# Performance work log

Hardware: AMD Instinct MI355X
Metric: run time of the kernel (lower is better)

## Reference

```python
import jax, jax.numpy as jnp
import numpy as np
from jax import lax

EPS = 1e-8


def setup_inputs() -> dict:
    key = jax.random.key(0)
    k1, k2, k3, k4, k5 = jax.random.split(key, 5)
    b, c_in, c_out, h, w_sp, k, z = 8, 256, 256, 128, 128, 3, 512
    return {
        "x": jax.random.normal(k1, (b, c_in, h, w_sp), dtype=jnp.float32),
        "w": jax.random.normal(k2, (b, z), dtype=jnp.float32),
        "weight": jax.random.normal(k3, (c_out, c_in, k, k), dtype=jnp.float32),
        "affine_w": jax.random.normal(k4, (c_in, z), dtype=jnp.float32) * 0.02,
        "affine_b": jax.random.normal(k5, (c_in,), dtype=jnp.float32) * 0.02,
    }


def reference(x, w, weight, affine_w, affine_b):
    # style: [b, c_in] -> broadcast over (out_ch, kh, kw); +1 as in StyleGAN2
    style = w @ affine_w.T + affine_b + 1.0                      # [b, c_in]
    wgt = weight[None] * style[:, None, :, None, None]           # [b, O, I, kh, kw]
    # demodulation
    denom = lax.rsqrt(jnp.sum(wgt * wgt, axis=(2, 3, 4)) + EPS)  # [b, O]
    wgt = wgt * denom[:, :, None, None, None]

    # per-sample conv (equivalent to groups=b grouped conv), 'same' padding
    def conv_one(xi, wi):
        # xi: [I, H, W], wi: [O, I, kh, kw]
        return lax.conv_general_dilated(
            xi[None], wi, window_strides=(1, 1), padding="SAME",
            dimension_numbers=("NCHW", "OIHW", "NCHW"))[0]

    return jax.vmap(conv_one)(x, wgt)                            # [b, O, H, W]
```

## Files before the change

kernel.cpp:

```cpp
#include <hip/hip_runtime.h>

#define EPS 1e-8f

using short8 = __attribute__((ext_vector_type(8))) short;
using f32x4  = __attribute__((ext_vector_type(4))) float;
typedef unsigned short u16;

__device__ __forceinline__ u16 f2bf(float f) {
    union { float f; unsigned u; } v; v.f = f;
    unsigned u = v.u;
    return (u16)((u + 0x7FFFu + ((u >> 16) & 1u)) >> 16);
}

__device__ __forceinline__ void g2l16(const void* gsrc, void* ldst) {
    __builtin_amdgcn_global_load_lds(
        (const __attribute__((address_space(1))) unsigned int*)gsrc,
        (__attribute__((address_space(3))) unsigned int*)ldst, 16, 0, 0);
}

__global__ void style_kernel(const float* __restrict__ w,
                             const float* __restrict__ affine_w,
                             const float* __restrict__ affine_b,
                             float* __restrict__ style) {
    int b = blockIdx.x;
    int i = threadIdx.x;
    __shared__ float wb[512];
    for (int z = threadIdx.x; z < 512; z += 256) wb[z] = w[b * 512 + z];
    __syncthreads();
    const float* aw = affine_w + i * 512;
    float acc = 0.f;
#pragma unroll 4
    for (int z = 0; z < 512; z += 4) {
        float4 a4 = *reinterpret_cast<const float4*>(aw + z);
        acc += a4.x * wb[z] + a4.y * wb[z + 1] + a4.z * wb[z + 2] + a4.w * wb[z + 3];
    }
    style[b * 256 + i] = acc + affine_b[i] + 1.0f;
}

__global__ void modw_kernel(const float* __restrict__ weight,
                            const float* __restrict__ style,
                            u16* __restrict__ wgt) {
    int b = blockIdx.x >> 8;
    int o = blockIdx.x & 255;
    int ic = threadIdx.x;
    float s = style[b * 256 + ic];
    const float* wp = weight + (size_t)(o * 256 + ic) * 9;
    float m[9];
    float ss = 0.f;
#pragma unroll
    for (int t = 0; t < 9; ++t) { m[t] = wp[t] * s; ss += m[t] * m[t]; }
#pragma unroll
    for (int off = 32; off > 0; off >>= 1) ss += __shfl_down(ss, off);
    __shared__ float part[4];
    int lane = threadIdx.x & 63, wid = threadIdx.x >> 6;
    if (lane == 0) part[wid] = ss;
    __syncthreads();
    float denom = rsqrtf(part[0] + part[1] + part[2] + part[3] + EPS);
    int g = ic >> 3, j = ic & 7;
#pragma unroll
    for (int t = 0; t < 9; ++t) {
        size_t idx = ((((size_t)(b * 9 + t) * 32 + g) * 256 + o) << 3) + j;
        wgt[idx] = f2bf(m[t] * denom);
    }
}

__global__ __launch_bounds__(256) void xform_kernel(const float* __restrict__ x,
                                                    u16* __restrict__ xb) {
    int s = blockIdx.x * 256 + threadIdx.x;
    int w = s & 127, h = (s >> 7) & 127, g = (s >> 14) & 31, b = s >> 19;
    const float* xp = x + (((size_t)(b * 256 + g * 8) * 128 + h) * 128 + w);
    union { u16 u[8]; short8 v; } pk;
#pragma unroll
    for (int j = 0; j < 8; ++j) pk.u[j] = f2bf(xp[(size_t)j * 16384]);
    *reinterpret_cast<short8*>(&xb[(size_t)s * 8]) = pk.v;
}

__global__ __launch_bounds__(256, 2) void conv_kernel(
    const u16* __restrict__ xb,
    const u16* __restrict__ wgt,
    float* __restrict__ out) {

    __shared__ __align__(16) u16 Xs[4][4][130][8];
    __shared__ __align__(16) u16 As[2][4][129][8];

    int bid = blockIdx.x;
    int ht = bid & 63;
    int ot = (bid >> 6) & 1;
    int b  = bid >> 7;
    int h0 = ht * 2;

    int tid = threadIdx.x, lane = tid & 63, wid = tid >> 6;
    int wm = wid >> 1, wr = wid & 1;
    int l15 = lane & 15, lg = lane >> 4;

    {
        short8 z = {0, 0, 0, 0, 0, 0, 0, 0};
        short8* xz = reinterpret_cast<short8*>(&Xs[0][0][0][0]);
        for (int i = tid; i < 2080; i += 256) xz[i] = z;
    }

    f32x4 acc[4][8] = {};

    auto stageX = [&](int c) {
        int hr = h0 + wid - 1;
        if ((unsigned)hr < 128u) {
#pragma unroll
            for (int k = 0; k < 8; ++k) {
                int g = k >> 1, half = k & 1;
                const u16* src = xb +
                    ((((size_t)(b * 32 + c * 4 + g) * 128 + hr) * 128) + half * 64 + lane) * 8;
                g2l16(src, &Xs[wid][g][1 + half * 64][0]);
            }
        }
    };
    auto stageA = [&](int nc, int nt, int nb) {
        const u16* base = wgt + ((((size_t)(b * 9 + nt) * 32) + nc * 4 + wid) * 256 + ot * 128) * 8;
        g2l16(base + (size_t)lane * 8, &As[nb][wid][0][0]);
        g2l16(base + (size_t)(64 + lane) * 8, &As[nb][wid][64][0]);
    };

    __syncthreads();
    stageX(0);
    stageA(0, 0, 0);
    __syncthreads();

    int cur = 0;
    for (int c = 0; c < 8; ++c) {
        for (int t = 0; t < 9; ++t) {
            bool lastPhase = (c == 7 && t == 8);
            if (!lastPhase) {
                int nt = t + 1, nc = c;
                if (nt == 9) { nt = 0; nc = c + 1; }
                stageA(nc, nt, cur ^ 1);
            }
            int kh = t / 3, kw = t - kh * 3;
            short8 af[4], bfv[8];
#pragma unroll
            for (int mi = 0; mi < 4; ++mi)
                af[mi] = *reinterpret_cast<const short8*>(&As[cur][lg][wm * 64 + mi * 16 + l15][0]);
#pragma unroll
            for (int ni = 0; ni < 8; ++ni)
                bfv[ni] = *reinterpret_cast<const short8*>(&Xs[wr + kh][lg][ni * 16 + l15 + kw][0]);
#pragma unroll
            for (int mi = 0; mi < 4; ++mi)
#pragma unroll
                for (int ni = 0; ni < 8; ++ni)
                    acc[mi][ni] = __builtin_amdgcn_mfma_f32_16x16x32_bf16(
                        af[mi], bfv[ni], acc[mi][ni], 0, 0, 0);
            if (t == 8 && c < 7) {
                __syncthreads();
                stageX(c + 1);
            }
            if (!lastPhase) __syncthreads();
            cur ^= 1;
        }
    }

    int h = h0 + wr;
#pragma unroll
    for (int mi = 0; mi < 4; ++mi) {
        int o = ot * 128 + wm * 64 + mi * 16 + lg * 4;
#pragma unroll
        for (int ni = 0; ni < 8; ++ni) {
            int w_ = ni * 16 + l15;
            float* op = out + (((size_t)(b * 256 + o) * 128 + h) * 128 + w_);
#pragma unroll
            for (int r = 0; r < 4; ++r)
                op[(size_t)r * 16384] = acc[mi][ni][r];
        }
    }
}

extern "C" void kernel_launch(void* const* d_in, const int* in_sizes, int n_in,
                              void* d_out, int out_size, void* d_ws, size_t ws_size,
                              hipStream_t stream) {
    const float* x        = (const float*)d_in[0];
    const float* w        = (const float*)d_in[1];
    const float* weight   = (const float*)d_in[2];
    const float* affine_w = (const float*)d_in[3];
    const float* affine_b = (const float*)d_in[4];
    float* out = (float*)d_out;

    float* style = (float*)d_ws;
    u16* wgt = (u16*)((char*)d_ws + 8192);
    u16* xbuf = (u16*)((char*)d_ws + 8192 + 9437184);

    xform_kernel<<<16384, 256, 0, stream>>>(x, xbuf);
    style_kernel<<<8, 256, 0, stream>>>(w, affine_w, affine_b, style);
    modw_kernel<<<2048, 256, 0, stream>>>(weight, style, wgt);
    conv_kernel<<<1024, 256, 0, stream>>>(xbuf, wgt, out);
}
```

Before: 202.7 us.

## Restructure conv kernel into 512-thread blocks with triple-buffered weights and double-buffered input

Each conv block now covers all 256 output channels with 8 waves, so every staged input row is reused across twice as many outputs. Weights move through a 3-deep LDS ring and input rows through a double buffer, and explicit vmcnt waits with one barrier per step replace the paired __syncthreads. The changes also add MFMA priority boosting, a block-index swizzle, and redirection of out-of-range row loads into a trash buffer. LDS use rises sharply, which may lower occupancy, and the hand-counted waits could be fragile.

```diff
diff --git a/kernel.cpp b/kernel.cpp
--- a/kernel.cpp
+++ b/kernel.cpp
@@ -5,6 +5,12 @@
 using short8 = __attribute__((ext_vector_type(8))) short;
 using f32x4  = __attribute__((ext_vector_type(4))) float;
 typedef unsigned short u16;
+
+#define WAITV(N) asm volatile("s_waitcnt vmcnt(" #N ")" ::: "memory")
+#define WAITLGKM0() do { asm volatile("s_waitcnt lgkmcnt(0)" ::: "memory"); \
+                         __builtin_amdgcn_sched_barrier(0); } while (0)
+#define BARRIER() do { __builtin_amdgcn_s_barrier(); \
+                       asm volatile("" ::: "memory"); } while (0)
 
 __device__ __forceinline__ u16 f2bf(float f) {
     union { float f; unsigned u; } v; v.f = f;
@@ -75,91 +81,103 @@
     *reinterpret_cast<short8*>(&xb[(size_t)s * 8]) = pk.v;
 }
 
-__global__ __launch_bounds__(256, 2) void conv_kernel(
+__global__ __launch_bounds__(512, 2) void conv_kernel(
     const u16* __restrict__ xb,
     const u16* __restrict__ wgt,
     float* __restrict__ out) {
 
-    __shared__ __align__(16) u16 Xs[4][4][130][8];
-    __shared__ __align__(16) u16 As[2][4][129][8];
+    __shared__ __align__(16) u16 Xs[2][4][4][130][8];
+    __shared__ __align__(16) u16 As[3][4][256][8];
+    __shared__ __align__(16) u16 trash[512];
 
     int bid = blockIdx.x;
-    int ht = bid & 63;
-    int ot = (bid >> 6) & 1;
-    int b  = bid >> 7;
+    int swz = (bid & 7) * 64 + (bid >> 3);
+    int ht = swz & 63, b = swz >> 6;
     int h0 = ht * 2;
 
     int tid = threadIdx.x, lane = tid & 63, wid = tid >> 6;
     int wm = wid >> 1, wr = wid & 1;
     int l15 = lane & 15, lg = lane >> 4;
 
+    auto stageA = [&](int p, int ring) {
+        int t = p % 9, c = p / 9;
+        const u16* wbase = wgt + ((size_t)(b * 9 + t) * 32 + c * 4) * (256 * 8);
+#pragma unroll
+        for (int k = 0; k < 2; ++k) {
+            int seg = wid * 2 + k, g = seg >> 2, oq = seg & 3;
+            const u16* src = wbase + ((size_t)g * 256 + oq * 64 + lane) * 8;
+            g2l16(src, &As[ring][g][oq * 64][0]);
+        }
+    };
+    auto stageX = [&](int c1, int bx) {
+        int row = wid >> 1;
+        int hr = h0 + row - 1;
+        bool oob = ((unsigned)hr >= 128u);
+        int hc = oob ? 0 : hr;
+#pragma unroll
+        for (int k = 0; k < 4; ++k) {
+            int g = (wid * 2 + (k >> 1)) & 3, half = k & 1;
+            const u16* src = xb +
+                ((((size_t)(b * 32 + c1 * 4 + g)) * 128 + hc) * 128 + half * 64 + lane) * 8;
+            void* dst = oob ? (void*)trash : (void*)&Xs[bx][row][g][1 + half * 64][0];
+            g2l16(src, dst);
+        }
+    };
+
     {
         short8 z = {0, 0, 0, 0, 0, 0, 0, 0};
-        short8* xz = reinterpret_cast<short8*>(&Xs[0][0][0][0]);
-        for (int i = tid; i < 2080; i += 256) xz[i] = z;
-    }
+        short8* p0 = reinterpret_cast<short8*>(&Xs[0][0][0][0][0]);
+        for (int i = tid; i < 4160; i += 512) p0[i] = z;
+    }
+    __syncthreads();
+
+    stageX(0, 0);
+    stageA(0, 0);
+    stageA(1, 1);
+    WAITV(2);
+    BARRIER();
 
     f32x4 acc[4][8] = {};
 
-    auto stageX = [&](int c) {
-        int hr = h0 + wid - 1;
-        if ((unsigned)hr < 128u) {
-#pragma unroll
-            for (int k = 0; k < 8; ++k) {
-                int g = k >> 1, half = k & 1;
-                const u16* src = xb +
-                    ((((size_t)(b * 32 + c * 4 + g) * 128 + hr) * 128) + half * 64 + lane) * 8;
-                g2l16(src, &Xs[wid][g][1 + half * 64][0]);
-            }
-        }
-    };
-    auto stageA = [&](int nc, int nt, int nb) {
-        const u16* base = wgt + ((((size_t)(b * 9 + nt) * 32) + nc * 4 + wid) * 256 + ot * 128) * 8;
-        g2l16(base + (size_t)lane * 8, &As[nb][wid][0][0]);
-        g2l16(base + (size_t)(64 + lane) * 8, &As[nb][wid][64][0]);
-    };
-
-    __syncthreads();
-    stageX(0);
-    stageA(0, 0, 0);
-    __syncthreads();
-
-    int cur = 0;
     for (int c = 0; c < 8; ++c) {
         for (int t = 0; t < 9; ++t) {
-            bool lastPhase = (c == 7 && t == 8);
-            if (!lastPhase) {
-                int nt = t + 1, nc = c;
-                if (nt == 9) { nt = 0; nc = c + 1; }
-                stageA(nc, nt, cur ^ 1);
-            }
+            int p = c * 9 + t;
+            if (t == 0 && c < 7) stageX(c + 1, (c + 1) & 1);
+            if (p <= 69) stageA(p + 2, (p + 2) % 3);
+
+            int ring = p % 3;
             int kh = t / 3, kw = t - kh * 3;
-            short8 af[4], bfv[8];
+            short8 af[4], bx8[8];
 #pragma unroll
             for (int mi = 0; mi < 4; ++mi)
-                af[mi] = *reinterpret_cast<const short8*>(&As[cur][lg][wm * 64 + mi * 16 + l15][0]);
+                af[mi] = *reinterpret_cast<const short8*>(
+                    &As[ring][lg][wm * 64 + mi * 16 + l15][0]);
 #pragma unroll
             for (int ni = 0; ni < 8; ++ni)
-                bfv[ni] = *reinterpret_cast<const short8*>(&Xs[wr + kh][lg][ni * 16 + l15 + kw][0]);
+                bx8[ni] = *reinterpret_cast<const short8*>(
+                    &Xs[c & 1][wr + kh][lg][ni * 16 + l15 + kw][0]);
+            WAITLGKM0();
+            __builtin_amdgcn_s_setprio(1);
 #pragma unroll
             for (int mi = 0; mi < 4; ++mi)
 #pragma unroll
                 for (int ni = 0; ni < 8; ++ni)
                     acc[mi][ni] = __builtin_amdgcn_mfma_f32_16x16x32_bf16(
-                        af[mi], bfv[ni], acc[mi][ni], 0, 0, 0);
-            if (t == 8 && c < 7) {
-                __syncthreads();
-                stageX(c + 1);
-            }
-            if (!lastPhase) __syncthreads();
-            cur ^= 1;
+                        af[mi], bx8[ni], acc[mi][ni], 0, 0, 0);
+            __builtin_amdgcn_s_setprio(0);
+            __builtin_amdgcn_sched_barrier(0);
+
+            if (t == 0 && c < 7)  { WAITV(6); }
+            else if (p <= 69)     { WAITV(2); }
+            else if (p == 70)     { WAITV(0); }
+            BARRIER();
         }
     }
 
     int h = h0 + wr;
 #pragma unroll
     for (int mi = 0; mi < 4; ++mi) {
-        int o = ot * 128 + wm * 64 + mi * 16 + lg * 4;
+        int o = wm * 64 + mi * 16 + lg * 4;
 #pragma unroll
         for (int ni = 0; ni < 8; ++ni) {
             int w_ = ni * 16 + l15;
@@ -188,5 +206,5 @@
     xform_kernel<<<16384, 256, 0, stream>>>(x, xbuf);
     style_kernel<<<8, 256, 0, stream>>>(w, affine_w, affine_b, style);
     modw_kernel<<<2048, 256, 0, stream>>>(weight, style, wgt);
-    conv_kernel<<<1024, 256, 0, stream>>>(xbuf, wgt, out);
-}
+    conv_kernel<<<512, 512, 0, stream>>>(xbuf, wgt, out);
+}
```

New measurement: 219.4 us. 1.08x slower.

## Drop LDS staging in conv; load fragments directly from padded global buffers

Applied to the files above, without the earlier changes.

The input transform now writes a zero-padded bf16 layout with halo rows and columns. The conv kernel loads MFMA operand fragments straight from global memory into registers, double-buffered one tap ahead, instead of staging through LDS with barriers. Each block now covers one output row for all 256 output channels, uses a swizzled block index, and raises wave priority around the MFMA loop. This removes LDS traffic and __syncthreads, at the cost of redundant global/L2 reads and more register pressure.

```diff
diff --git a/kernel.cpp b/kernel.cpp
--- a/kernel.cpp
+++ b/kernel.cpp
@@ -10,12 +10,6 @@
     union { float f; unsigned u; } v; v.f = f;
     unsigned u = v.u;
     return (u16)((u + 0x7FFFu + ((u >> 16) & 1u)) >> 16);
-}
-
-__device__ __forceinline__ void g2l16(const void* gsrc, void* ldst) {
-    __builtin_amdgcn_global_load_lds(
-        (const __attribute__((address_space(1))) unsigned int*)gsrc,
-        (__attribute__((address_space(3))) unsigned int*)ldst, 16, 0, 0);
 }
 
 __global__ void style_kernel(const float* __restrict__ w,
@@ -66,13 +60,20 @@
 
 __global__ __launch_bounds__(256) void xform_kernel(const float* __restrict__ x,
                                                     u16* __restrict__ xb) {
+    int r = blockIdx.y;
     int s = blockIdx.x * 256 + threadIdx.x;
-    int w = s & 127, h = (s >> 7) & 127, g = (s >> 14) & 31, b = s >> 19;
-    const float* xp = x + (((size_t)(b * 256 + g * 8) * 128 + h) * 128 + w);
+    if (s >= 4160) return;
+    int g = s / 130, wp = s - g * 130;
+    short8* dst = reinterpret_cast<short8*>(xb + ((size_t)r * 4160 + s) * 8);
+    short8 z = {0, 0, 0, 0, 0, 0, 0, 0};
+    if (r == 0) { *dst = z; return; }
+    int b = (r - 1) / 129, hh = (r - 1) - b * 129;
+    if (hh == 128 || wp == 0 || wp == 129) { *dst = z; return; }
+    const float* xp = x + (((size_t)(b * 256 + g * 8)) * 128 + hh) * 128 + (wp - 1);
     union { u16 u[8]; short8 v; } pk;
 #pragma unroll
     for (int j = 0; j < 8; ++j) pk.u[j] = f2bf(xp[(size_t)j * 16384]);
-    *reinterpret_cast<short8*>(&xb[(size_t)s * 8]) = pk.v;
+    *dst = pk.v;
 }
 
 __global__ __launch_bounds__(256, 2) void conv_kernel(
@@ -80,86 +81,69 @@
     const u16* __restrict__ wgt,
     float* __restrict__ out) {
 
-    __shared__ __align__(16) u16 Xs[4][4][130][8];
-    __shared__ __align__(16) u16 As[2][4][129][8];
+    int bid = blockIdx.x;
+    int swz = ((bid & 7) << 7) | (bid >> 3);
+    int h = swz & 127, b = swz >> 7;
 
-    int bid = blockIdx.x;
-    int ht = bid & 63;
-    int ot = (bid >> 6) & 1;
-    int b  = bid >> 7;
-    int h0 = ht * 2;
-
-    int tid = threadIdx.x, lane = tid & 63, wid = tid >> 6;
-    int wm = wid >> 1, wr = wid & 1;
+    int tid = threadIdx.x, lane = tid & 63, og = tid >> 6;
     int l15 = lane & 15, lg = lane >> 4;
 
-    {
-        short8 z = {0, 0, 0, 0, 0, 0, 0, 0};
-        short8* xz = reinterpret_cast<short8*>(&Xs[0][0][0][0]);
-        for (int i = tid; i < 2080; i += 256) xz[i] = z;
-    }
+    const int RP = 33280;
+    int lanePartA = lg * 2048 + og * 512 + l15 * 8;
+    int lanePartB = lg * 1040 + l15 * 8;
 
+    short8 af[2][4], bx[2][8];
     f32x4 acc[4][8] = {};
 
-    auto stageX = [&](int c) {
-        int hr = h0 + wid - 1;
-        if ((unsigned)hr < 128u) {
+    auto issueA = [&](int buf, int c, int t) {
+        const u16* ap = wgt + (size_t)((b * 9 + t) * 32 + c * 4) * 2048 + lanePartA;
 #pragma unroll
-            for (int k = 0; k < 8; ++k) {
-                int g = k >> 1, half = k & 1;
-                const u16* src = xb +
-                    ((((size_t)(b * 32 + c * 4 + g) * 128 + hr) * 128) + half * 64 + lane) * 8;
-                g2l16(src, &Xs[wid][g][1 + half * 64][0]);
-            }
-        }
+        for (int mi = 0; mi < 4; ++mi)
+            af[buf][mi] = *reinterpret_cast<const short8*>(ap + mi * 128);
     };
-    auto stageA = [&](int nc, int nt, int nb) {
-        const u16* base = wgt + ((((size_t)(b * 9 + nt) * 32) + nc * 4 + wid) * 256 + ot * 128) * 8;
-        g2l16(base + (size_t)lane * 8, &As[nb][wid][0][0]);
-        g2l16(base + (size_t)(64 + lane) * 8, &As[nb][wid][64][0]);
+    auto issueB = [&](int buf, int c, int t) {
+        int kh = t / 3, kw = t - kh * 3;
+        const u16* bp = xb + (size_t)(b * 129 + h + kh) * RP + c * 4160 +
+                        lanePartB + kw * 8;
+#pragma unroll
+        for (int ni = 0; ni < 8; ++ni)
+            bx[buf][ni] = *reinterpret_cast<const short8*>(bp + ni * 128);
+    };
+    auto domfma = [&](int cur) {
+        __builtin_amdgcn_s_setprio(1);
+#pragma unroll
+        for (int mi = 0; mi < 4; ++mi)
+#pragma unroll
+            for (int ni = 0; ni < 8; ++ni)
+                acc[mi][ni] = __builtin_amdgcn_mfma_f32_16x16x32_bf16(
+                    af[cur][mi], bx[cur][ni], acc[cur == cur ? mi : mi][ni], 0, 0, 0);
+        __builtin_amdgcn_s_setprio(0);
     };
 
-    __syncthreads();
-    stageX(0);
-    stageA(0, 0, 0);
-    __syncthreads();
-
-    int cur = 0;
-    for (int c = 0; c < 8; ++c) {
-        for (int t = 0; t < 9; ++t) {
-            bool lastPhase = (c == 7 && t == 8);
-            if (!lastPhase) {
-                int nt = t + 1, nc = c;
-                if (nt == 9) { nt = 0; nc = c + 1; }
-                stageA(nc, nt, cur ^ 1);
+    issueA(0, 0, 0);
+    issueB(0, 0, 0);
+#pragma unroll 1
+    for (int c2 = 0; c2 < 8; c2 += 2) {
+#pragma unroll
+        for (int tt = 0; tt < 18; ++tt) {
+            int cur = tt & 1;
+            bool last = (c2 == 6) && (tt == 17);
+            if (!last) {
+                int ntt = tt + 1;
+                int nc, nt;
+                if (ntt == 18) { nc = c2 + 2; nt = 0; }
+                else if (ntt >= 9) { nc = c2 + 1; nt = ntt - 9; }
+                else { nc = c2; nt = ntt; }
+                issueA(cur ^ 1, nc, nt);
+                issueB(cur ^ 1, nc, nt);
             }
-            int kh = t / 3, kw = t - kh * 3;
-            short8 af[4], bfv[8];
-#pragma unroll
-            for (int mi = 0; mi < 4; ++mi)
-                af[mi] = *reinterpret_cast<const short8*>(&As[cur][lg][wm * 64 + mi * 16 + l15][0]);
-#pragma unroll
-            for (int ni = 0; ni < 8; ++ni)
-                bfv[ni] = *reinterpret_cast<const short8*>(&Xs[wr + kh][lg][ni * 16 + l15 + kw][0]);
-#pragma unroll
-            for (int mi = 0; mi < 4; ++mi)
-#pragma unroll
-                for (int ni = 0; ni < 8; ++ni)
-                    acc[mi][ni] = __builtin_amdgcn_mfma_f32_16x16x32_bf16(
-                        af[mi], bfv[ni], acc[mi][ni], 0, 0, 0);
-            if (t == 8 && c < 7) {
-                __syncthreads();
-                stageX(c + 1);
-            }
-            if (!lastPhase) __syncthreads();
-            cur ^= 1;
+            domfma(cur);
         }
     }
 
-    int h = h0 + wr;
 #pragma unroll
     for (int mi = 0; mi < 4; ++mi) {
-        int o = ot * 128 + wm * 64 + mi * 16 + lg * 4;
+        int o = og * 64 + mi * 16 + lg * 4;
 #pragma unroll
         for (int ni = 0; ni < 8; ++ni) {
             int w_ = ni * 16 + l15;
@@ -185,7 +169,7 @@
     u16* wgt = (u16*)((char*)d_ws + 8192);
     u16* xbuf = (u16*)((char*)d_ws + 8192 + 9437184);
 
-    xform_kernel<<<16384, 256, 0, stream>>>(x, xbuf);
+    xform_kernel<<<dim3(17, 1033), 256, 0, stream>>>(x, xbuf);
     style_kernel<<<8, 256, 0, stream>>>(w, affine_w, affine_b, style);
     modw_kernel<<<2048, 256, 0, stream>>>(weight, style, wgt);
     conv_kernel<<<1024, 256, 0, stream>>>(xbuf, wgt, out);
```

New measurement: 235.1 us. 16.0% more time.
